# Kernel optimization log

Hardware: AMD Instinct MI355X
Metric: run time of the kernel (lower is better)

The kernel has to match this reference:

```python
import jax, jax.numpy as jnp
import numpy as np

EMBED_DIM = 1024
HEADS = 16
HEAD_DIM = EMBED_DIM // HEADS


def setup_inputs() -> dict:
    key = jax.random.key(0)
    ks = jax.random.split(key, 9)
    D = EMBED_DIM
    s = 1.0 / np.sqrt(D)
    x = jax.random.normal(ks[0], (4, 2048, D), dtype=jnp.float32)
    Wq = jax.random.uniform(ks[1], (D, D), jnp.float32, -s, s)
    bq = jnp.zeros((D,), jnp.float32)
    Wk = jax.random.uniform(ks[2], (D, D), jnp.float32, -s, s)
    bk = jnp.zeros((D,), jnp.float32)
    Wv = jax.random.uniform(ks[3], (D, D), jnp.float32, -s, s)
    bv = jnp.zeros((D,), jnp.float32)
    Wo = jax.random.uniform(ks[4], (D, D), jnp.float32, -s, s)
    bo = jnp.zeros((D,), jnp.float32)
    gamma = jnp.ones((D,), jnp.float32)
    beta = jnp.zeros((D,), jnp.float32)
    return {"x": x, "Wq": Wq, "bq": bq, "Wk": Wk, "bk": bk,
            "Wv": Wv, "bv": bv, "Wo": Wo, "bo": bo,
            "gamma": gamma, "beta": beta}


def reference(x, Wq, bq, Wk, bk, Wv, bv, Wo, bo, gamma, beta):
    B, S, D = x.shape
    H, Dh = HEADS, HEAD_DIM
    # projections -> [B, H, S, Dh]
    q = (x @ Wq + bq).reshape(B, S, H, Dh).transpose(0, 2, 1, 3)
    k = (x @ Wk + bk).reshape(B, S, H, Dh).transpose(0, 2, 1, 3)
    v = (x @ Wv + bv).reshape(B, S, H, Dh).transpose(0, 2, 1, 3)
    scores = jnp.einsum('bhqd,bhkd->bhqk', q, k) / jnp.sqrt(jnp.float32(Dh))
    attn = jax.nn.softmax(scores, axis=-1)  # dropout is identity in eval
    ctx = jnp.einsum('bhqk,bhkd->bhqd', attn, v)
    ctx = ctx.transpose(0, 2, 1, 3).reshape(B, S, D)
    out = ctx @ Wo + bo
    # residual + LayerNorm (eps=1e-5, torch default)
    h = out + x
    mu = jnp.mean(h, axis=-1, keepdims=True)
    var = jnp.mean(jnp.square(h - mu), axis=-1, keepdims=True)
    return (h - mu) * jax.lax.rsqrt(var + 1e-5) * gamma + beta
```

## Files before the change

### kernel.cpp

```cpp
#include <hip/hip_runtime.h>
#include <hip/hip_bf16.h>
#include <stdint.h>

typedef short sh4 __attribute__((ext_vector_type(4)));
typedef short sh8 __attribute__((ext_vector_type(8)));
typedef float fl4 __attribute__((ext_vector_type(4)));
typedef float f32x4 __attribute__((ext_vector_type(4)));
typedef float f32x16 __attribute__((ext_vector_type(16)));
typedef uint32_t u32x4 __attribute__((ext_vector_type(4)));

static __device__ __forceinline__ short f2bf(float f) {
  union { float f; uint32_t u; } v;
  v.f = f;
  uint32_t r = v.u + 0x7fffu + ((v.u >> 16) & 1u);
  return (short)(r >> 16);
}

static __device__ __forceinline__ uint32_t cvt_pk_bf16(float a, float b) {
  uint32_t r;
  asm("v_cvt_pk_bf16_f32 %0, %1, %2" : "=v"(r) : "v"(a), "v"(b));
  return r;
}

static __device__ __forceinline__ void pl32swap(uint32_t& a, uint32_t& b) {
  asm volatile("v_permlane32_swap_b32 %0, %1" : "+v"(a), "+v"(b));
}

static __device__ __forceinline__ void gload_lds16(const void* g, void* l) {
  __builtin_amdgcn_global_load_lds((const __attribute__((address_space(1))) void*)g,
                                   (__attribute__((address_space(3))) void*)l, 16, 0, 0);
}

__global__ __launch_bounds__(256) void k_wt(const float* __restrict__ Wq, const float* __restrict__ Wk,
                                            const float* __restrict__ Wv, const float* __restrict__ Wo,
                                            short* __restrict__ Tq, short* __restrict__ Tk,
                                            short* __restrict__ Tv, short* __restrict__ To) {
  const float* W = blockIdx.z == 0 ? Wq : blockIdx.z == 1 ? Wk : blockIdx.z == 2 ? Wv : Wo;
  short* T = blockIdx.z == 0 ? Tq : blockIdx.z == 1 ? Tk : blockIdx.z == 2 ? Tv : To;
  __shared__ float tile[32][33];
  int n0 = blockIdx.x * 32, k0 = blockIdx.y * 32;
  int tx = threadIdx.x, ty = threadIdx.y;
#pragma unroll
  for (int p = 0; p < 4; p++) tile[ty + 8 * p][tx] = W[(size_t)(k0 + ty + 8 * p) * 1024 + n0 + tx];
  __syncthreads();
#pragma unroll
  for (int p = 0; p < 4; p++) T[(size_t)(n0 + ty + 8 * p) * 1024 + k0 + tx] = f2bf(tile[tx][ty + 8 * p]);
}

__global__ __launch_bounds__(256) void k_cvtx(const float* __restrict__ x, short* __restrict__ o) {
  int i = blockIdx.x * 256 + threadIdx.x;
  fl4 v = ((const fl4*)x)[i];
  sh4 r;
#pragma unroll
  for (int j = 0; j < 4; j++) r[j] = f2bf(v[j]);
  ((sh4*)o)[i] = r;
}

__global__ __launch_bounds__(256) void k_qkv3(const short* __restrict__ A, const short* __restrict__ WT3,
                                              const float* __restrict__ bq, const float* __restrict__ bk,
                                              const float* __restrict__ bv, short* __restrict__ Qo,
                                              short* __restrict__ Ko, short* __restrict__ Vo, float qscale) {
  __shared__ __align__(16) short As[2][128 * 32];
  __shared__ __align__(16) short Bs[2][128 * 32];
  const int xcd = blockIdx.x & 7, j = blockIdx.x >> 3;
  const int m0 = (xcd + 8 * (j & 7)) * 128, n0 = (j >> 3) * 128;
  const int sec = n0 >> 10;
  const float* bias = sec == 0 ? bq : sec == 1 ? bk : bv;
  short* Out = sec == 0 ? Qo : sec == 1 ? Ko : Vo;
  const float scale = sec == 0 ? qscale : 1.f;
  const bool tr = (sec != 2);
  const int t = threadIdx.x;
  const int lane = t & 63, w = t >> 6;
  const int wr = w >> 1, wc = w & 1;
  const int l15 = lane & 15, g = lane >> 4;
  f32x4 acc[4][4];
#pragma unroll
  for (int mi = 0; mi < 4; mi++)
#pragma unroll
    for (int ni = 0; ni < 4; ni++) acc[mi][ni] = (f32x4){0.f, 0.f, 0.f, 0.f};

  auto stage = [&](int kk, int buf) {
    int r0 = w * 32;
#pragma unroll
    for (int i = 0; i < 2; i++) {
      int row = r0 + i * 16 + (lane >> 2);
      gload_lds16(&A[(size_t)(m0 + row) * 1024 + kk + (lane & 3) * 8], &As[buf][(r0 + i * 16) * 32]);
      gload_lds16(&WT3[(size_t)(n0 + row) * 1024 + kk + (lane & 3) * 8], &Bs[buf][(r0 + i * 16) * 32]);
    }
  };

  stage(0, 0);
  __syncthreads();
  for (int it = 0; it < 32; it++) {
    int buf = it & 1;
    if (it + 1 < 32) stage((it + 1) * 32, buf ^ 1);
    sh8 a[4], b[4];
#pragma unroll
    for (int i = 0; i < 4; i++) a[i] = *(sh8*)&As[buf][(wr * 64 + i * 16 + l15) * 32 + g * 8];
#pragma unroll
    for (int i = 0; i < 4; i++) b[i] = *(sh8*)&Bs[buf][(wc * 64 + i * 16 + l15) * 32 + g * 8];
    __builtin_amdgcn_s_setprio(1);
    if (tr) {
#pragma unroll
      for (int mi = 0; mi < 4; mi++)
#pragma unroll
        for (int ni = 0; ni < 4; ni++)
          acc[mi][ni] = __builtin_amdgcn_mfma_f32_16x16x32_bf16(b[ni], a[mi], acc[mi][ni], 0, 0, 0);
    } else {
#pragma unroll
      for (int mi = 0; mi < 4; mi++)
#pragma unroll
        for (int ni = 0; ni < 4; ni++)
          acc[mi][ni] = __builtin_amdgcn_mfma_f32_16x16x32_bf16(a[mi], b[ni], acc[mi][ni], 0, 0, 0);
    }
    __builtin_amdgcn_s_setprio(0);
    __syncthreads();
  }
  if (tr) {
#pragma unroll
    for (int ni = 0; ni < 4; ni++) {
      int nbase = n0 + wc * 64 + ni * 16 + g * 4;
      int nn0 = nbase & 1023;
      fl4 bv4 = *(const fl4*)&bias[nn0];
      int h = nn0 >> 6, dh0 = nn0 & 63;
#pragma unroll
      for (int mi = 0; mi < 4; mi++) {
        int m = m0 + wr * 64 + mi * 16 + l15;
        int bb = m >> 11, s = m & 2047;
        uint2 dd;
        dd.x = cvt_pk_bf16((acc[mi][ni][0] + bv4[0]) * scale, (acc[mi][ni][1] + bv4[1]) * scale);
        dd.y = cvt_pk_bf16((acc[mi][ni][2] + bv4[2]) * scale, (acc[mi][ni][3] + bv4[3]) * scale);
        *(uint2*)&Out[(((size_t)bb * 16 + h) * 2048 + s) * 64 + dh0] = dd;
      }
    }
  } else {
#pragma unroll
    for (int ni = 0; ni < 4; ni++) {
      int col = n0 + wc * 64 + ni * 16 + l15;
      int nn = col & 1023;
      float bvv = bias[nn];
      int h = nn >> 6, dh = nn & 63;
#pragma unroll
      for (int mi = 0; mi < 4; mi++) {
        int mr = m0 + wr * 64 + mi * 16 + g * 4;
        int bb = mr >> 11, s = mr & 2047;
        uint2 dd;
        dd.x = cvt_pk_bf16(acc[mi][ni][0] + bvv, acc[mi][ni][1] + bvv);
        dd.y = cvt_pk_bf16(acc[mi][ni][2] + bvv, acc[mi][ni][3] + bvv);
        *(uint2*)&Vo[(((size_t)bb * 16 + h) * 64 + dh) * 2048 + s] = dd;
      }
    }
  }
}

__global__ __launch_bounds__(256) void k_oproj(const short* __restrict__ A, const short* __restrict__ BT,
                                               const float* __restrict__ bias, const float* __restrict__ X,
                                               float* __restrict__ Out) {
  __shared__ __align__(16) short As[2][128 * 32];
  __shared__ __align__(16) short Bs[2][128 * 32];
  const int xcd = blockIdx.x & 7, j = blockIdx.x >> 3;
  const int m0 = (xcd + 8 * (j & 7)) * 128, n0 = (j >> 3) * 128;
  const int t = threadIdx.x;
  const int lane = t & 63, w = t >> 6;
  const int wr = w >> 1, wc = w & 1;
  const int l15 = lane & 15, g = lane >> 4;
  f32x4 acc[4][4];
#pragma unroll
  for (int mi = 0; mi < 4; mi++)
#pragma unroll
    for (int ni = 0; ni < 4; ni++) acc[mi][ni] = (f32x4){0.f, 0.f, 0.f, 0.f};

  auto stage = [&](int kk, int buf) {
    int r0 = w * 32;
#pragma unroll
    for (int i = 0; i < 2; i++) {
      int row = r0 + i * 16 + (lane >> 2);
      gload_lds16(&A[(size_t)(m0 + row) * 1024 + kk + (lane & 3) * 8], &As[buf][(r0 + i * 16) * 32]);
      gload_lds16(&BT[(size_t)(n0 + row) * 1024 + kk + (lane & 3) * 8], &Bs[buf][(r0 + i * 16) * 32]);
    }
  };

  stage(0, 0);
  __syncthreads();
  for (int it = 0; it < 32; it++) {
    int buf = it & 1;
    if (it + 1 < 32) stage((it + 1) * 32, buf ^ 1);
    sh8 a[4], b[4];
#pragma unroll
    for (int i = 0; i < 4; i++) a[i] = *(sh8*)&As[buf][(wr * 64 + i * 16 + l15) * 32 + g * 8];
#pragma unroll
    for (int i = 0; i < 4; i++) b[i] = *(sh8*)&Bs[buf][(wc * 64 + i * 16 + l15) * 32 + g * 8];
    __builtin_amdgcn_s_setprio(1);
#pragma unroll
    for (int mi = 0; mi < 4; mi++)
#pragma unroll
      for (int ni = 0; ni < 4; ni++)
        acc[mi][ni] = __builtin_amdgcn_mfma_f32_16x16x32_bf16(b[ni], a[mi], acc[mi][ni], 0, 0, 0);
    __builtin_amdgcn_s_setprio(0);
    __syncthreads();
  }
#pragma unroll
  for (int ni = 0; ni < 4; ni++) {
    int nbase = n0 + wc * 64 + ni * 16 + g * 4;
    fl4 bv4 = *(const fl4*)&bias[nbase];
#pragma unroll
    for (int mi = 0; mi < 4; mi++) {
      int m = m0 + wr * 64 + mi * 16 + l15;
      fl4 xv = *(const fl4*)&X[(size_t)m * 1024 + nbase];
      fl4 r;
#pragma unroll
      for (int e = 0; e < 4; e++) r[e] = acc[mi][ni][e] + bv4[e] + xv[e];
      *(fl4*)&Out[(size_t)m * 1024 + nbase] = r;
    }
  }
}

__global__ __launch_bounds__(256, 3) void k_attn(const short* __restrict__ Q, const short* __restrict__ K,
                                                 const short* __restrict__ Vt, short* __restrict__ CTX) {
  const int nid = (blockIdx.x & 7) * 128 + (blockIdx.x >> 3);
  const int qb = nid & 15, h = (nid >> 4) & 15, b = nid >> 8;
  const int q0 = qb * 128;
  const size_t ho = (((size_t)b * 16 + h) * 2048) * 64;
  const short* Qh = Q + ho;
  const short* Kh = K + ho;
  const short* Vh = Vt + ho;
  __shared__ __align__(16) short Ks[2][64 * 64];
  __shared__ __align__(16) short Vs[2][64 * 64];
  const int t = threadIdx.x, lane = t & 63, w = t >> 6;
  const int l31 = lane & 31, hi = lane >> 5;
  const int swz = (l31 & 7) << 4;
  const float MSHIFT = -12.f;

  sh8 qreg[4];
#pragma unroll
  for (int ks = 0; ks < 4; ks++)
    qreg[ks] = *(const sh8*)&Qh[(size_t)(q0 + w * 32 + l31) * 64 + ks * 16 + hi * 8];

  f32x16 oc0, oc1;
#pragma unroll
  for (int r = 0; r < 16; r++) { oc0[r] = 0.f; oc1[r] = 0.f; }
  float l_s = 0.f;

  auto stage = [&](int kt, int buf) {
    int r0 = w * 16;
#pragma unroll
    for (int i = 0; i < 2; i++) {
      int row = r0 + i * 8 + (lane >> 3);
      int colb = ((lane & 7) * 16) ^ ((row & 7) << 4);
      gload_lds16(&Kh[(size_t)(kt * 64 + row) * 64 + (colb >> 1)], &Ks[buf][(r0 + i * 8) * 64]);
      gload_lds16(&Vh[(size_t)row * 2048 + kt * 64 + (colb >> 1)], &Vs[buf][(r0 + i * 8) * 64]);
    }
  };

  stage(0, 0);
  __syncthreads();

  for (int kt = 0; kt < 32; kt++) {
    int buf = kt & 1;
    if (kt + 1 < 32) stage(kt + 1, buf ^ 1);

    f32x16 s0, s1;
#pragma unroll
    for (int r = 0; r < 16; r++) { s0[r] = MSHIFT; s1[r] = MSHIFT; }
    __builtin_amdgcn_s_setprio(1);
#pragma unroll
    for (int ks = 0; ks < 4; ks++) {
      sh8 ak0 = *(sh8*)((char*)&Ks[buf][0] + l31 * 128 + ((ks * 32 + hi * 16) ^ swz));
      sh8 ak1 = *(sh8*)((char*)&Ks[buf][0] + (32 + l31) * 128 + ((ks * 32 + hi * 16) ^ swz));
      s0 = __builtin_amdgcn_mfma_f32_32x32x16_bf16(ak0, qreg[ks], s0, 0, 0, 0);
      s1 = __builtin_amdgcn_mfma_f32_32x32x16_bf16(ak1, qreg[ks], s1, 0, 0, 0);
    }
    __builtin_amdgcn_s_setprio(0);

    float ps = 0.f;
#pragma unroll
    for (int r = 0; r < 16; r++) { s0[r] = __builtin_amdgcn_exp2f(s0[r]); ps += s0[r]; }
#pragma unroll
    for (int r = 0; r < 16; r++) { s1[r] = __builtin_amdgcn_exp2f(s1[r]); ps += s1[r]; }
    l_s += ps;

    u32x4 pw0, pw1, pw2, pw3;
    {
      uint32_t a0 = cvt_pk_bf16(s0[0], s0[1]), a1 = cvt_pk_bf16(s0[2], s0[3]);
      uint32_t b0 = cvt_pk_bf16(s0[4], s0[5]), b1 = cvt_pk_bf16(s0[6], s0[7]);
      uint32_t c0 = cvt_pk_bf16(s0[8], s0[9]), c1 = cvt_pk_bf16(s0[10], s0[11]);
      uint32_t d0 = cvt_pk_bf16(s0[12], s0[13]), d1 = cvt_pk_bf16(s0[14], s0[15]);
      pl32swap(a0, b0); pl32swap(a1, b1); pl32swap(c0, d0); pl32swap(c1, d1);
      pw0 = (u32x4){a0, a1, b0, b1};
      pw1 = (u32x4){c0, c1, d0, d1};
      a0 = cvt_pk_bf16(s1[0], s1[1]); a1 = cvt_pk_bf16(s1[2], s1[3]);
      b0 = cvt_pk_bf16(s1[4], s1[5]); b1 = cvt_pk_bf16(s1[6], s1[7]);
      c0 = cvt_pk_bf16(s1[8], s1[9]); c1 = cvt_pk_bf16(s1[10], s1[11]);
      d0 = cvt_pk_bf16(s1[12], s1[13]); d1 = cvt_pk_bf16(s1[14], s1[15]);
      pl32swap(a0, b0); pl32swap(a1, b1); pl32swap(c0, d0); pl32swap(c1, d1);
      pw2 = (u32x4){a0, a1, b0, b1};
      pw3 = (u32x4){c0, c1, d0, d1};
    }
    sh8 pb0 = __builtin_bit_cast(sh8, pw0), pb1 = __builtin_bit_cast(sh8, pw1);
    sh8 pb2 = __builtin_bit_cast(sh8, pw2), pb3 = __builtin_bit_cast(sh8, pw3);

    __builtin_amdgcn_s_setprio(1);
#pragma unroll
    for (int ks = 0; ks < 4; ks++) {
      sh8 pb = ks == 0 ? pb0 : ks == 1 ? pb1 : ks == 2 ? pb2 : pb3;
      sh8 av0 = *(sh8*)((char*)&Vs[buf][0] + l31 * 128 + ((ks * 32 + hi * 16) ^ swz));
      sh8 av1 = *(sh8*)((char*)&Vs[buf][0] + (32 + l31) * 128 + ((ks * 32 + hi * 16) ^ swz));
      oc0 = __builtin_amdgcn_mfma_f32_32x32x16_bf16(av0, pb, oc0, 0, 0, 0);
      oc1 = __builtin_amdgcn_mfma_f32_32x32x16_bf16(av1, pb, oc1, 0, 0, 0);
    }
    __builtin_amdgcn_s_setprio(0);
    __syncthreads();
  }

  l_s += __shfl_xor(l_s, 32);
  float li = 1.f / l_s;
  int s = q0 + w * 32 + l31;
  size_t obase = (((size_t)b * 2048 + s) * 16 + h) * 64;
#pragma unroll
  for (int rq = 0; rq < 4; rq++) {
    uint2 dd;
    dd.x = cvt_pk_bf16(oc0[4 * rq] * li, oc0[4 * rq + 1] * li);
    dd.y = cvt_pk_bf16(oc0[4 * rq + 2] * li, oc0[4 * rq + 3] * li);
    *(uint2*)&CTX[obase + rq * 8 + hi * 4] = dd;
    dd.x = cvt_pk_bf16(oc1[4 * rq] * li, oc1[4 * rq + 1] * li);
    dd.y = cvt_pk_bf16(oc1[4 * rq + 2] * li, oc1[4 * rq + 3] * li);
    *(uint2*)&CTX[obase + 32 + rq * 8 + hi * 4] = dd;
  }
}

__global__ __launch_bounds__(256) void k_ln(float* __restrict__ Out, const float* __restrict__ gamma,
                                            const float* __restrict__ beta) {
  int row = blockIdx.x * 4 + (threadIdx.x >> 6);
  int lane = threadIdx.x & 63;
  float* p = Out + (size_t)row * 1024;
  fl4 v[4];
  float s = 0.f, s2 = 0.f;
#pragma unroll
  for (int j = 0; j < 4; j++) {
    v[j] = *(fl4*)&p[lane * 4 + j * 256];
#pragma unroll
    for (int e = 0; e < 4; e++) { s += v[j][e]; s2 += v[j][e] * v[j][e]; }
  }
#pragma unroll
  for (int off = 1; off < 64; off <<= 1) {
    s += __shfl_xor(s, off);
    s2 += __shfl_xor(s2, off);
  }
  float mu = s * (1.f / 1024.f);
  float var = s2 * (1.f / 1024.f) - mu * mu;
  float inv = rsqrtf(var + 1e-5f);
#pragma unroll
  for (int j = 0; j < 4; j++) {
    fl4 r;
#pragma unroll
    for (int e = 0; e < 4; e++) {
      int c = lane * 4 + j * 256 + e;
      r[e] = (v[j][e] - mu) * inv * gamma[c] + beta[c];
    }
    *(fl4*)&p[lane * 4 + j * 256] = r;
  }
}

extern "C" void kernel_launch(void* const* d_in, const int* in_sizes, int n_in,
                              void* d_out, int out_size, void* d_ws, size_t ws_size,
                              hipStream_t stream) {
  (void)in_sizes; (void)n_in; (void)out_size; (void)ws_size;
  const float* x = (const float*)d_in[0];
  const float* Wq = (const float*)d_in[1];
  const float* bq = (const float*)d_in[2];
  const float* Wk = (const float*)d_in[3];
  const float* bk = (const float*)d_in[4];
  const float* Wv = (const float*)d_in[5];
  const float* bv = (const float*)d_in[6];
  const float* Wo = (const float*)d_in[7];
  const float* bo = (const float*)d_in[8];
  const float* gamma = (const float*)d_in[9];
  const float* beta = (const float*)d_in[10];
  float* out = (float*)d_out;
  char* ws = (char*)d_ws;
  short* xbf = (short*)(ws);
  short* wtq = (short*)(ws + (16ull << 20));
  short* wtk = (short*)(ws + (18ull << 20));
  short* wtv = (short*)(ws + (20ull << 20));
  short* wto = (short*)(ws + (22ull << 20));
  short* qb  = (short*)(ws + (24ull << 20));
  short* kbuf = (short*)(ws + (40ull << 20));
  short* vbuf = (short*)(ws + (56ull << 20));
  short* ctx = (short*)(ws + (72ull << 20));

  const float QSCALE = 0.125f * 1.44269504088896f;

  k_wt<<<dim3(32, 32, 4), dim3(32, 8), 0, stream>>>(Wq, Wk, Wv, Wo, wtq, wtk, wtv, wto);
  k_cvtx<<<8192, 256, 0, stream>>>(x, xbf);
  k_qkv3<<<1536, 256, 0, stream>>>(xbf, wtq, bq, bk, bv, qb, kbuf, vbuf, QSCALE);
  k_attn<<<1024, 256, 0, stream>>>(qb, kbuf, vbuf, ctx);
  k_oproj<<<512, 256, 0, stream>>>(ctx, wto, bo, x, out);
  k_ln<<<2048, 256, 0, stream>>>(out, gamma, beta);
}
```

Baseline: 235.8 us.

## Deepen GEMM pipeline to four LDS buffers and split QKV into QK and V kernels

The projection GEMMs move from a double-buffered loop, which issues a full __syncthreads per k-step, to a four-buffer ring with prefetch distance two. Each step uses an explicit vmcnt wait and a single s_barrier, so global-to-LDS loads overlap more of the MFMA work. The fused QKV kernel is split into a Q/K kernel and a separate V kernel, so each has a fixed operand order and epilogue with no runtime branch. In exchange, LDS per block doubles to 64KB, which may lower occupancy, and there is one extra kernel launch.

```diff
diff --git a/kernel.cpp b/kernel.cpp
--- a/kernel.cpp
+++ b/kernel.cpp
@@ -56,19 +56,35 @@
   ((sh4*)o)[i] = r;
 }
 
-__global__ __launch_bounds__(256) void k_qkv3(const short* __restrict__ A, const short* __restrict__ WT3,
-                                              const float* __restrict__ bq, const float* __restrict__ bk,
-                                              const float* __restrict__ bv, short* __restrict__ Qo,
-                                              short* __restrict__ Ko, short* __restrict__ Vo, float qscale) {
-  __shared__ __align__(16) short As[2][128 * 32];
-  __shared__ __align__(16) short Bs[2][128 * 32];
+
+#define GEMM_PIPE_LOOP(STAGE_BODY, COMPUTE_BODY)                         \
+  STAGE_BODY(0, 0);                                                      \
+  STAGE_BODY(1, 1);                                                      \
+  for (int it = 0; it < 32; it++) {                                      \
+    if (it + 2 < 32) { int sb = (it + 2) & 3; STAGE_BODY(it + 2, sb); }  \
+    if (it < 30)                                                         \
+      asm volatile("s_waitcnt vmcnt(8)" ::: "memory");                   \
+    else if (it == 30)                                                   \
+      asm volatile("s_waitcnt vmcnt(4)" ::: "memory");                   \
+    else                                                                 \
+      asm volatile("s_waitcnt vmcnt(0)" ::: "memory");                   \
+    __builtin_amdgcn_s_barrier();                                        \
+    __builtin_amdgcn_sched_barrier(0);                                   \
+    { int buf = it & 3; COMPUTE_BODY }                                   \
+    asm volatile("" ::: "memory");                                       \
+  }
+
+__global__ __launch_bounds__(256) void k_qk(const short* __restrict__ A, const short* __restrict__ WT2,
+                                            const float* __restrict__ bq, const float* __restrict__ bk,
+                                            short* __restrict__ Qo, short* __restrict__ Ko, float qscale) {
+  __shared__ __align__(16) short As[4][128 * 32];
+  __shared__ __align__(16) short Bs[4][128 * 32];
   const int xcd = blockIdx.x & 7, j = blockIdx.x >> 3;
   const int m0 = (xcd + 8 * (j & 7)) * 128, n0 = (j >> 3) * 128;
   const int sec = n0 >> 10;
-  const float* bias = sec == 0 ? bq : sec == 1 ? bk : bv;
-  short* Out = sec == 0 ? Qo : sec == 1 ? Ko : Vo;
+  const float* bias = sec == 0 ? bq : bk;
+  short* Out = sec == 0 ? Qo : Ko;
   const float scale = sec == 0 ? qscale : 1.f;
-  const bool tr = (sec != 2);
   const int t = threadIdx.x;
   const int lane = t & 63, w = t >> 6;
   const int wr = w >> 1, wc = w & 1;
@@ -79,85 +95,52 @@
 #pragma unroll
     for (int ni = 0; ni < 4; ni++) acc[mi][ni] = (f32x4){0.f, 0.f, 0.f, 0.f};
 
-  auto stage = [&](int kk, int buf) {
-    int r0 = w * 32;
-#pragma unroll
-    for (int i = 0; i < 2; i++) {
-      int row = r0 + i * 16 + (lane >> 2);
-      gload_lds16(&A[(size_t)(m0 + row) * 1024 + kk + (lane & 3) * 8], &As[buf][(r0 + i * 16) * 32]);
-      gload_lds16(&WT3[(size_t)(n0 + row) * 1024 + kk + (lane & 3) * 8], &Bs[buf][(r0 + i * 16) * 32]);
-    }
-  };
-
-  stage(0, 0);
-  __syncthreads();
-  for (int it = 0; it < 32; it++) {
-    int buf = it & 1;
-    if (it + 1 < 32) stage((it + 1) * 32, buf ^ 1);
-    sh8 a[4], b[4];
-#pragma unroll
-    for (int i = 0; i < 4; i++) a[i] = *(sh8*)&As[buf][(wr * 64 + i * 16 + l15) * 32 + g * 8];
-#pragma unroll
-    for (int i = 0; i < 4; i++) b[i] = *(sh8*)&Bs[buf][(wc * 64 + i * 16 + l15) * 32 + g * 8];
-    __builtin_amdgcn_s_setprio(1);
-    if (tr) {
-#pragma unroll
-      for (int mi = 0; mi < 4; mi++)
-#pragma unroll
-        for (int ni = 0; ni < 4; ni++)
+#define QK_STAGE(kt, buf)                                                                     \
+  {                                                                                           \
+    int r0 = w * 32;                                                                          \
+    _Pragma("unroll") for (int i = 0; i < 2; i++) {                                           \
+      int row = r0 + i * 16 + (lane >> 2);                                                    \
+      gload_lds16(&A[(size_t)(m0 + row) * 1024 + (kt) * 32 + (lane & 3) * 8],                 \
+                  &As[buf][(r0 + i * 16) * 32]);                                              \
+      gload_lds16(&WT2[(size_t)(n0 + row) * 1024 + (kt) * 32 + (lane & 3) * 8],               \
+                  &Bs[buf][(r0 + i * 16) * 32]);                                              \
+    }                                                                                         \
+  }
+
+#define QK_COMPUTE                                                                            \
+  sh8 a[4], b[4];                                                                             \
+  _Pragma("unroll") for (int i = 0; i < 4; i++)                                               \
+      a[i] = *(sh8*)&As[buf][(wr * 64 + i * 16 + l15) * 32 + g * 8];                          \
+  _Pragma("unroll") for (int i = 0; i < 4; i++)                                               \
+      b[i] = *(sh8*)&Bs[buf][(wc * 64 + i * 16 + l15) * 32 + g * 8];                          \
+  _Pragma("unroll") for (int mi = 0; mi < 4; mi++)                                            \
+      _Pragma("unroll") for (int ni = 0; ni < 4; ni++)                                        \
           acc[mi][ni] = __builtin_amdgcn_mfma_f32_16x16x32_bf16(b[ni], a[mi], acc[mi][ni], 0, 0, 0);
-    } else {
-#pragma unroll
-      for (int mi = 0; mi < 4; mi++)
-#pragma unroll
-        for (int ni = 0; ni < 4; ni++)
-          acc[mi][ni] = __builtin_amdgcn_mfma_f32_16x16x32_bf16(a[mi], b[ni], acc[mi][ni], 0, 0, 0);
-    }
-    __builtin_amdgcn_s_setprio(0);
-    __syncthreads();
-  }
-  if (tr) {
-#pragma unroll
-    for (int ni = 0; ni < 4; ni++) {
-      int nbase = n0 + wc * 64 + ni * 16 + g * 4;
-      int nn0 = nbase & 1023;
-      fl4 bv4 = *(const fl4*)&bias[nn0];
-      int h = nn0 >> 6, dh0 = nn0 & 63;
-#pragma unroll
-      for (int mi = 0; mi < 4; mi++) {
-        int m = m0 + wr * 64 + mi * 16 + l15;
-        int bb = m >> 11, s = m & 2047;
-        uint2 dd;
-        dd.x = cvt_pk_bf16((acc[mi][ni][0] + bv4[0]) * scale, (acc[mi][ni][1] + bv4[1]) * scale);
-        dd.y = cvt_pk_bf16((acc[mi][ni][2] + bv4[2]) * scale, (acc[mi][ni][3] + bv4[3]) * scale);
-        *(uint2*)&Out[(((size_t)bb * 16 + h) * 2048 + s) * 64 + dh0] = dd;
-      }
-    }
-  } else {
-#pragma unroll
-    for (int ni = 0; ni < 4; ni++) {
-      int col = n0 + wc * 64 + ni * 16 + l15;
-      int nn = col & 1023;
-      float bvv = bias[nn];
-      int h = nn >> 6, dh = nn & 63;
-#pragma unroll
-      for (int mi = 0; mi < 4; mi++) {
-        int mr = m0 + wr * 64 + mi * 16 + g * 4;
-        int bb = mr >> 11, s = mr & 2047;
-        uint2 dd;
-        dd.x = cvt_pk_bf16(acc[mi][ni][0] + bvv, acc[mi][ni][1] + bvv);
-        dd.y = cvt_pk_bf16(acc[mi][ni][2] + bvv, acc[mi][ni][3] + bvv);
-        *(uint2*)&Vo[(((size_t)bb * 16 + h) * 64 + dh) * 2048 + s] = dd;
-      }
-    }
-  }
-}
-
-__global__ __launch_bounds__(256) void k_oproj(const short* __restrict__ A, const short* __restrict__ BT,
-                                               const float* __restrict__ bias, const float* __restrict__ X,
-                                               float* __restrict__ Out) {
-  __shared__ __align__(16) short As[2][128 * 32];
-  __shared__ __align__(16) short Bs[2][128 * 32];
+
+  GEMM_PIPE_LOOP(QK_STAGE, QK_COMPUTE)
+
+#pragma unroll
+  for (int ni = 0; ni < 4; ni++) {
+    int nbase = n0 + wc * 64 + ni * 16 + g * 4;
+    int nn0 = nbase & 1023;
+    fl4 bv4 = *(const fl4*)&bias[nn0];
+    int h = nn0 >> 6, dh0 = nn0 & 63;
+#pragma unroll
+    for (int mi = 0; mi < 4; mi++) {
+      int m = m0 + wr * 64 + mi * 16 + l15;
+      int bb = m >> 11, s = m & 2047;
+      uint2 dd;
+      dd.x = cvt_pk_bf16((acc[mi][ni][0] + bv4[0]) * scale, (acc[mi][ni][1] + bv4[1]) * scale);
+      dd.y = cvt_pk_bf16((acc[mi][ni][2] + bv4[2]) * scale, (acc[mi][ni][3] + bv4[3]) * scale);
+      *(uint2*)&Out[(((size_t)bb * 16 + h) * 2048 + s) * 64 + dh0] = dd;
+    }
+  }
+}
+
+__global__ __launch_bounds__(256) void k_v(const short* __restrict__ A, const short* __restrict__ WTv,
+                                           const float* __restrict__ bv, short* __restrict__ Vo) {
+  __shared__ __align__(16) short As[4][128 * 32];
+  __shared__ __align__(16) short Bs[4][128 * 32];
   const int xcd = blockIdx.x & 7, j = blockIdx.x >> 3;
   const int m0 = (xcd + 8 * (j & 7)) * 128, n0 = (j >> 3) * 128;
   const int t = threadIdx.x;
@@ -170,35 +153,89 @@
 #pragma unroll
     for (int ni = 0; ni < 4; ni++) acc[mi][ni] = (f32x4){0.f, 0.f, 0.f, 0.f};
 
-  auto stage = [&](int kk, int buf) {
-    int r0 = w * 32;
-#pragma unroll
-    for (int i = 0; i < 2; i++) {
-      int row = r0 + i * 16 + (lane >> 2);
-      gload_lds16(&A[(size_t)(m0 + row) * 1024 + kk + (lane & 3) * 8], &As[buf][(r0 + i * 16) * 32]);
-      gload_lds16(&BT[(size_t)(n0 + row) * 1024 + kk + (lane & 3) * 8], &Bs[buf][(r0 + i * 16) * 32]);
-    }
-  };
-
-  stage(0, 0);
-  __syncthreads();
-  for (int it = 0; it < 32; it++) {
-    int buf = it & 1;
-    if (it + 1 < 32) stage((it + 1) * 32, buf ^ 1);
-    sh8 a[4], b[4];
-#pragma unroll
-    for (int i = 0; i < 4; i++) a[i] = *(sh8*)&As[buf][(wr * 64 + i * 16 + l15) * 32 + g * 8];
-#pragma unroll
-    for (int i = 0; i < 4; i++) b[i] = *(sh8*)&Bs[buf][(wc * 64 + i * 16 + l15) * 32 + g * 8];
-    __builtin_amdgcn_s_setprio(1);
-#pragma unroll
-    for (int mi = 0; mi < 4; mi++)
-#pragma unroll
-      for (int ni = 0; ni < 4; ni++)
-        acc[mi][ni] = __builtin_amdgcn_mfma_f32_16x16x32_bf16(b[ni], a[mi], acc[mi][ni], 0, 0, 0);
-    __builtin_amdgcn_s_setprio(0);
-    __syncthreads();
-  }
+#define V_STAGE(kt, buf)                                                                      \
+  {                                                                                           \
+    int r0 = w * 32;                                                                          \
+    _Pragma("unroll") for (int i = 0; i < 2; i++) {                                           \
+      int row = r0 + i * 16 + (lane >> 2);                                                    \
+      gload_lds16(&A[(size_t)(m0 + row) * 1024 + (kt) * 32 + (lane & 3) * 8],                 \
+                  &As[buf][(r0 + i * 16) * 32]);                                              \
+      gload_lds16(&WTv[(size_t)(n0 + row) * 1024 + (kt) * 32 + (lane & 3) * 8],               \
+                  &Bs[buf][(r0 + i * 16) * 32]);                                              \
+    }                                                                                         \
+  }
+
+#define V_COMPUTE                                                                             \
+  sh8 a[4], b[4];                                                                             \
+  _Pragma("unroll") for (int i = 0; i < 4; i++)                                               \
+      a[i] = *(sh8*)&As[buf][(wr * 64 + i * 16 + l15) * 32 + g * 8];                          \
+  _Pragma("unroll") for (int i = 0; i < 4; i++)                                               \
+      b[i] = *(sh8*)&Bs[buf][(wc * 64 + i * 16 + l15) * 32 + g * 8];                          \
+  _Pragma("unroll") for (int mi = 0; mi < 4; mi++)                                            \
+      _Pragma("unroll") for (int ni = 0; ni < 4; ni++)                                        \
+          acc[mi][ni] = __builtin_amdgcn_mfma_f32_16x16x32_bf16(a[mi], b[ni], acc[mi][ni], 0, 0, 0);
+
+  GEMM_PIPE_LOOP(V_STAGE, V_COMPUTE)
+
+#pragma unroll
+  for (int ni = 0; ni < 4; ni++) {
+    int col = n0 + wc * 64 + ni * 16 + l15;
+    int nn = col & 1023;
+    float bvv = bv[nn];
+    int h = nn >> 6, dh = nn & 63;
+#pragma unroll
+    for (int mi = 0; mi < 4; mi++) {
+      int mr = m0 + wr * 64 + mi * 16 + g * 4;
+      int bb = mr >> 11, s = mr & 2047;
+      uint2 dd;
+      dd.x = cvt_pk_bf16(acc[mi][ni][0] + bvv, acc[mi][ni][1] + bvv);
+      dd.y = cvt_pk_bf16(acc[mi][ni][2] + bvv, acc[mi][ni][3] + bvv);
+      *(uint2*)&Vo[(((size_t)bb * 16 + h) * 64 + dh) * 2048 + s] = dd;
+    }
+  }
+}
+
+__global__ __launch_bounds__(256) void k_oproj(const short* __restrict__ A, const short* __restrict__ BT,
+                                               const float* __restrict__ bias, const float* __restrict__ X,
+                                               float* __restrict__ Out) {
+  __shared__ __align__(16) short As[4][128 * 32];
+  __shared__ __align__(16) short Bs[4][128 * 32];
+  const int xcd = blockIdx.x & 7, j = blockIdx.x >> 3;
+  const int m0 = (xcd + 8 * (j & 7)) * 128, n0 = (j >> 3) * 128;
+  const int t = threadIdx.x;
+  const int lane = t & 63, w = t >> 6;
+  const int wr = w >> 1, wc = w & 1;
+  const int l15 = lane & 15, g = lane >> 4;
+  f32x4 acc[4][4];
+#pragma unroll
+  for (int mi = 0; mi < 4; mi++)
+#pragma unroll
+    for (int ni = 0; ni < 4; ni++) acc[mi][ni] = (f32x4){0.f, 0.f, 0.f, 0.f};
+
+#define O_STAGE(kt, buf)                                                                      \
+  {                                                                                           \
+    int r0 = w * 32;                                                                          \
+    _Pragma("unroll") for (int i = 0; i < 2; i++) {                                           \
+      int row = r0 + i * 16 + (lane >> 2);                                                    \
+      gload_lds16(&A[(size_t)(m0 + row) * 1024 + (kt) * 32 + (lane & 3) * 8],                 \
+                  &As[buf][(r0 + i * 16) * 32]);                                              \
+      gload_lds16(&BT[(size_t)(n0 + row) * 1024 + (kt) * 32 + (lane & 3) * 8],                \
+                  &Bs[buf][(r0 + i * 16) * 32]);                                              \
+    }                                                                                         \
+  }
+
+#define O_COMPUTE                                                                             \
+  sh8 a[4], b[4];                                                                             \
+  _Pragma("unroll") for (int i = 0; i < 4; i++)                                               \
+      a[i] = *(sh8*)&As[buf][(wr * 64 + i * 16 + l15) * 32 + g * 8];                          \
+  _Pragma("unroll") for (int i = 0; i < 4; i++)                                               \
+      b[i] = *(sh8*)&Bs[buf][(wc * 64 + i * 16 + l15) * 32 + g * 8];                          \
+  _Pragma("unroll") for (int mi = 0; mi < 4; mi++)                                            \
+      _Pragma("unroll") for (int ni = 0; ni < 4; ni++)                                        \
+          acc[mi][ni] = __builtin_amdgcn_mfma_f32_16x16x32_bf16(b[ni], a[mi], acc[mi][ni], 0, 0, 0);
+
+  GEMM_PIPE_LOOP(O_STAGE, O_COMPUTE)
+
 #pragma unroll
   for (int ni = 0; ni < 4; ni++) {
     int nbase = n0 + wc * 64 + ni * 16 + g * 4;
@@ -392,7 +429,8 @@
 
   k_wt<<<dim3(32, 32, 4), dim3(32, 8), 0, stream>>>(Wq, Wk, Wv, Wo, wtq, wtk, wtv, wto);
   k_cvtx<<<8192, 256, 0, stream>>>(x, xbf);
-  k_qkv3<<<1536, 256, 0, stream>>>(xbf, wtq, bq, bk, bv, qb, kbuf, vbuf, QSCALE);
+  k_qk<<<1024, 256, 0, stream>>>(xbf, wtq, bq, bk, qb, kbuf, QSCALE);
+  k_v<<<512, 256, 0, stream>>>(xbf, wtv, bv, vbuf);
   k_attn<<<1024, 256, 0, stream>>>(qb, kbuf, vbuf, ctx);
   k_oproj<<<512, 256, 0, stream>>>(ctx, wto, bo, x, out);
   k_ln<<<2048, 256, 0, stream>>>(out, gamma, beta);
```

Measured after the change: 217.8 us. 7.6% less time.
